# Kernel tuning notes

Measured on AMD Instinct MI355X. Metric: run time of the kernel, lower is better.

The kernel has to match this reference:

```python
import jax, jax.numpy as jnp
import numpy as np

NUM_HEADS = 8
HEAD_DIM = 64
AVG_K_LENGTH = 20
SCALE = 1.0 / (HEAD_DIM ** 0.5 * float(np.log(AVG_K_LENGTH)))  # 1/(sqrt(dim)*log(avg_k_length))


def setup_inputs() -> dict:
    key = jax.random.key(0)
    k1, k2, k3, k4 = jax.random.split(key, 4)
    B, HD, LQ, LK = 4, NUM_HEADS * HEAD_DIM, 2048, 2048
    q = jax.random.normal(k1, (B, HD, LQ), dtype=jnp.float32)
    k = jax.random.normal(k2, (B, HD, LK), dtype=jnp.float32)
    v = jax.random.normal(k3, (B, HD, LK), dtype=jnp.float32)
    k_length = jax.random.randint(k4, (B,), 512, LK + 1, dtype=jnp.int32)
    return {"q": q, "k": k, "v": v, "k_length": k_length}


def reference(q, k, v, k_length):
    b, hd, lq = q.shape
    lk = k.shape[-1]
    d = hd // NUM_HEADS
    # b (h d) l -> b h d l
    qh = q.reshape(b, NUM_HEADS, d, lq)
    kh = k.reshape(b, NUM_HEADS, d, lk)
    vh = v.reshape(b, NUM_HEADS, d, lk)
    # per-batch entropy-invariance scale: scale * log(k_length)
    s = SCALE * jnp.log(k_length.astype(jnp.float32))[:, None, None, None]  # (b,1,1,1)
    attn = jnp.einsum('bhdq,bhdk->bhqk', qh, kh)  # (b,h,lq,lk)
    attn = jax.nn.softmax(s * attn, axis=-1)
    out = jnp.einsum('bhqk,bhdk->bhdq', attn, vh)  # (b,h,d,lq)
    return out.reshape(b, hd, lq)
```

## Files before the change

### kernel.cpp

```cpp
#include <hip/hip_runtime.h>
#include <hip/hip_bf16.h>
#include <math.h>


typedef __attribute__((ext_vector_type(8))) short short8_t;
typedef __attribute__((ext_vector_type(4))) short short4_t;
typedef __attribute__((ext_vector_type(4))) float float4_t;

#define SEQ   2048
#define NBH   32
#define NKT   32

__device__ __forceinline__ unsigned f2bf2u(float a, float b) {
#if __has_builtin(__builtin_amdgcn_cvt_pk_bf16_f32)
  typedef __bf16 bf16x2_t __attribute__((ext_vector_type(2)));
  union { bf16x2_t v; unsigned u; } cv;
  cv.v = __builtin_amdgcn_cvt_pk_bf16_f32(a, b);
  return cv.u;
#else
  union { float f; unsigned u; } x, y;
  x.f = a; y.f = b;
  unsigned ra = x.u + 0x7fffu + ((x.u >> 16) & 1u);
  unsigned rb = y.u + 0x7fffu + ((y.u >> 16) & 1u);
  return (ra >> 16) | (rb & 0xffff0000u);
#endif
}

__device__ __forceinline__ short f2bf1(float a) {
  return (short)(f2bf2u(a, a) & 0xffffu);
}

__device__ __forceinline__ float fast_exp2(float x) {
#if __has_builtin(__builtin_amdgcn_exp2f)
  return __builtin_amdgcn_exp2f(x);
#else
  return exp2f(x);
#endif
}

__device__ __forceinline__ void gld16(const void* g, void* l) {
  __builtin_amdgcn_global_load_lds(
      (const __attribute__((address_space(1))) void*)g,
      (__attribute__((address_space(3))) void*)l, 16, 0, 0);
}

__device__ __forceinline__ float4_t mfma32(short8_t a, short8_t b, float4_t c) {
  return __builtin_amdgcn_mfma_f32_16x16x32_bf16(a, b, c, 0, 0, 0);
}

__device__ __forceinline__ float4_t mfma16(short4_t a, short4_t b, float4_t c) {
#if __has_builtin(__builtin_amdgcn_mfma_f32_16x16x16bf16_1k)
  return __builtin_amdgcn_mfma_f32_16x16x16bf16_1k(a, b, c, 0, 0, 0);
#else
  asm("v_mfma_f32_16x16x16_bf16 %0, %1, %2, %0" : "+v"(c) : "v"(a), "v"(b));
  return c;
#endif
}

#define PST 68
__global__ __launch_bounds__(256, 8)
void eia_prep_kernel(const float* __restrict__ kg, const float* __restrict__ vg,
                     unsigned short* __restrict__ Kt2, unsigned short* __restrict__ Vt2) {
  __shared__ __align__(16) short T[64 * PST];
  const int id  = blockIdx.x;
  const int isV = id >> 10;
  const int sub = id & 1023;
  const int bh  = sub >> 5;
  const int kt  = sub & 31;
  const int t   = threadIdx.x;

  if (!isV) {
    const size_t ib = ((size_t)bh * 64) * SEQ + (size_t)(kt * 64) + (t & 63);
    const int dg = t >> 6;
#pragma unroll
    for (int dd = 0; dd < 16; dd += 4) {
      const int d = dg * 16 + dd;
      const float f0 = kg[ib + (size_t)(d + 0) * SEQ];
      const float f1 = kg[ib + (size_t)(d + 1) * SEQ];
      const float f2 = kg[ib + (size_t)(d + 2) * SEQ];
      const float f3 = kg[ib + (size_t)(d + 3) * SEQ];
      union { short4_t s; unsigned u[2]; } p;
      p.u[0] = f2bf2u(f0, f1);
      p.u[1] = f2bf2u(f2, f3);
      *(short4_t*)&T[(t & 63) * PST + d] = p.s;
    }
    __syncthreads();
    unsigned short* outt = Kt2 + (size_t)(bh * 32 + kt) * 4096;
#pragma unroll
    for (int rep = 0; rep < 2; ++rep) {
      const int id2 = rep * 256 + t;
      const int lr = id2 & 63, ch = id2 >> 6;
      union { short8_t v; short4_t h[2]; } o;
      o.h[0] = *(const short4_t*)&T[lr * PST + ch * 8];
      o.h[1] = *(const short4_t*)&T[lr * PST + ch * 8 + 4];
      *(short8_t*)&outt[ch * 512 + lr * 8] = o.v;
    }
  } else {
#pragma unroll
    for (int rep = 0; rep < 4; ++rep) {
      const int id2 = rep * 256 + t;
      const int d = id2 >> 4, l4 = (id2 & 15) * 4;
      const float4_t f = *(const float4_t*)&vg[((size_t)bh * 64 + d) * SEQ + kt * 64 + l4];
      union { short4_t s; unsigned u[2]; } p;
      p.u[0] = f2bf2u(f[0], f[1]);
      p.u[1] = f2bf2u(f[2], f[3]);
      *(short4_t*)&T[d * PST + l4] = p.s;
    }
    __syncthreads();
    unsigned short* outt = Vt2 + (size_t)(bh * 32 + kt) * 4096;
#pragma unroll
    for (int rep = 0; rep < 2; ++rep) {
      const int c = rep * 256 + t;
      const int k4 = c >> 5, dp = c & 31;
      union { short8_t v; short4_t h[2]; } o;
      o.h[0] = *(const short4_t*)&T[(2 * dp) * PST + k4 * 4];
      o.h[1] = *(const short4_t*)&T[(2 * dp + 1) * PST + k4 * 4];
      *(short8_t*)&outt[k4 * 256 + dp * 8] = o.v;
    }
  }
}

__global__ __launch_bounds__(128, 2)
void eia_attn_kernel(const float* __restrict__ qg,
                     const unsigned short* __restrict__ Kt2,
                     const unsigned short* __restrict__ Vt2,
                     const int* __restrict__ klen,
                     float* __restrict__ outg) {
  __shared__ __align__(16) short SM[16384];

  const int tid  = threadIdx.x;
  const int bh   = blockIdx.x & 31;
  const int qt   = blockIdx.x >> 5;
  const int q0   = qt * 64;
  const int w    = tid >> 6;
  const int lane = tid & 63;
  const int quad = lane >> 4;
  const int l16  = lane & 15;

  const float c = (1.4426950408889634f / (8.0f * 2.9957322735539909f)) *
                  logf((float)klen[bh >> 3]);
  const size_t qb = (size_t)bh * 64 * SEQ;

#pragma unroll
  for (int rep = 0; rep < 8; ++rep) {
    const int id = rep * 128 + tid;
    const int d  = id >> 4;
    const int q4 = (id & 15) * 4;
    const float4_t f = *(const float4_t*)&qg[qb + (size_t)d * SEQ + (size_t)(q0 + q4)];
    SM[(q4 + 0) * 68 + d] = f2bf1(c * f[0]);
    SM[(q4 + 1) * 68 + d] = f2bf1(c * f[1]);
    SM[(q4 + 2) * 68 + d] = f2bf1(c * f[2]);
    SM[(q4 + 3) * 68 + d] = f2bf1(c * f[3]);
  }
  __syncthreads();

  short8_t qfrag[2][2];
#pragma unroll
  for (int g = 0; g < 2; ++g)
#pragma unroll
    for (int s = 0; s < 2; ++s) {
      const short* qp = &SM[(w * 32 + g * 16 + l16) * 68 + s * 32 + quad * 8];
      const short4_t lo = *(const short4_t*)qp;
      const short4_t hi = *(const short4_t*)(qp + 4);
      qfrag[g][s] = short8_t{lo[0], lo[1], lo[2], lo[3], hi[0], hi[1], hi[2], hi[3]};
    }
  __syncthreads();

  const char* ksrc = (const char*)Kt2 + (size_t)bh * NKT * 8192 + w * 4096 + lane * 16;
  const char* vsrc = (const char*)Vt2 + (size_t)bh * NKT * 8192 + w * 4096 + lane * 16;
  short* const kdst = &SM[w * 2048 + lane * 8];
  short* const vdst = &SM[8192 + w * 2048 + lane * 8];

  const short* const kfp = &SM[quad * 512 + l16 * 8];
  const short* const vfp = &SM[8192 + quad * 256 + l16 * 4];

  const float4_t z4 = {0.f, 0.f, 0.f, 0.f};
  float4_t oacc[2][4];
#pragma unroll
  for (int g = 0; g < 2; ++g)
#pragma unroll
    for (int tt = 0; tt < 4; ++tt) oacc[g][tt] = z4;
  float4_t lacc[2] = {z4, z4};
  const short one_bf = (short)0x3F80;
  const short4_t ones4 = (l16 == 0) ? short4_t{one_bf, one_bf, one_bf, one_bf}
                                    : short4_t{0, 0, 0, 0};

#pragma unroll
  for (int i = 0; i < 4; ++i) gld16(ksrc + i * 1024, kdst + i * 512);
#pragma unroll
  for (int i = 0; i < 4; ++i) gld16(vsrc + i * 1024, vdst + i * 512);
  size_t goff = 8192;

#pragma unroll 2
  for (int kt = 0; kt < NKT; ++kt) {
    __syncthreads();

    if (kt < NKT - 1) {
      const int pn = ((kt + 1) & 1) * 4096;
#pragma unroll
      for (int i = 0; i < 4; ++i) gld16(ksrc + goff + i * 1024, kdst + pn + i * 512);
#pragma unroll
      for (int i = 0; i < 4; ++i) gld16(vsrc + goff + i * 1024, vdst + pn + i * 512);
      goff += 8192;
    }
    const int par = (kt & 1) * 4096;

    float4_t sac[2][4];
#pragma unroll
    for (int t = 0; t < 4; ++t) {
      const short8_t kv = *(const short8_t*)(kfp + par + t * 128);
      sac[0][t] = mfma32(kv, qfrag[0][0], z4);
      sac[1][t] = mfma32(kv, qfrag[1][0], z4);
    }
#pragma unroll
    for (int t = 0; t < 4; ++t) {
      const short8_t kv = *(const short8_t*)(kfp + par + 2048 + t * 128);
      sac[0][t] = mfma32(kv, qfrag[0][1], sac[0][t]);
      sac[1][t] = mfma32(kv, qfrag[1][1], sac[1][t]);
    }

    short4_t pbf[2][4];
#pragma unroll
    for (int g = 0; g < 2; ++g)
#pragma unroll
      for (int t = 0; t < 4; ++t) {
        const float e0 = fast_exp2(sac[g][t][0]);
        const float e1 = fast_exp2(sac[g][t][1]);
        const float e2 = fast_exp2(sac[g][t][2]);
        const float e3 = fast_exp2(sac[g][t][3]);
        union { short4_t s; unsigned u[2]; } p;
        p.u[0] = f2bf2u(e0, e1);
        p.u[1] = f2bf2u(e2, e3);
        pbf[g][t] = p.s;
        lacc[g] = mfma16(ones4, pbf[g][t], lacc[g]);
      }

#pragma unroll
    for (int t = 0; t < 4; ++t) {
      const short* vfb = vfp + par + t * 1024;
#pragma unroll
      for (int tt = 0; tt < 4; ++tt) {
        const short4_t vv = *(const short4_t*)(vfb + tt * 64);
        oacc[0][tt] = mfma16(vv, pbf[0][t], oacc[0][tt]);
        oacc[1][tt] = mfma16(vv, pbf[1][t], oacc[1][tt]);
      }
    }
  }

#pragma unroll
  for (int g = 0; g < 2; ++g) {
    const float ls  = __shfl(lacc[g][0], l16, 64);
    const float inv = 1.0f / ls;
    const size_t ob = qb + (size_t)(q0 + w * 32 + g * 16 + l16);
#pragma unroll
    for (int tt = 0; tt < 4; ++tt)
#pragma unroll
      for (int r = 0; r < 4; ++r)
        outg[ob + (size_t)(tt * 16 + quad * 4 + r) * SEQ] = oacc[g][tt][r] * inv;
  }
}

#define DPAD  72
#define PPAD  68
__global__ __launch_bounds__(256, 5)
void eia_attn_fb(const float* __restrict__ qg, const float* __restrict__ kg,
                 const float* __restrict__ vg, const int* __restrict__ klen,
                 float* __restrict__ outg) {
  __shared__ __align__(16) short QPs[64 * DPAD];
  __shared__ __align__(16) short Ksf[64 * DPAD];
  __shared__ __align__(16) short Vsf[64 * DPAD];

  const int tid  = threadIdx.x;
  const int bh   = blockIdx.x & 31;
  const int qt   = blockIdx.x >> 5;
  const int q0   = qt * 64;
  const int w    = tid >> 6;
  const int lane = tid & 63;
  const int quad = lane >> 4;
  const int l16  = lane & 15;

  const size_t base = (size_t)bh * 64 * SEQ;
  const float c = (1.4426950408889634f / (8.0f * 2.9957322735539909f)) *
                  logf((float)klen[bh >> 3]);

#pragma unroll
  for (int it = 0; it < 2; ++it) {
    const int e = it * 4 + w;
    float f[8];
#pragma unroll
    for (int j = 0; j < 8; ++j)
      f[j] = c * qg[base + (size_t)(e * 8 + j) * SEQ + (size_t)(q0 + lane)];
    union { short8_t s8; unsigned u[4]; } t;
#pragma unroll
    for (int j = 0; j < 4; ++j) t.u[j] = f2bf2u(f[2 * j], f[2 * j + 1]);
    *(short8_t*)&QPs[lane * DPAD + e * 8] = t.s8;
  }
  __syncthreads();

  short8_t qfrag[2];
#pragma unroll
  for (int s = 0; s < 2; ++s)
    qfrag[s] = *(const short8_t*)&QPs[(w * 16 + l16) * DPAD + s * 32 + quad * 8];

  float4_t oacc[4];
#pragma unroll
  for (int t = 0; t < 4; ++t) { oacc[t][0] = 0.f; oacc[t][1] = 0.f; oacc[t][2] = 0.f; oacc[t][3] = 0.f; }
  float lsumv[4] = {0.f, 0.f, 0.f, 0.f};
  const int pbase = w * (16 * DPAD);

  for (int kt = 0; kt < NKT; ++kt) {
    const int k0 = kt * 64;
#pragma unroll
    for (int it = 0; it < 2; ++it) {
      float f[8];
#pragma unroll
      for (int j = 0; j < 8; ++j)
        f[j] = kg[base + (size_t)((it * 4 + w) * 8 + j) * SEQ + (size_t)(k0 + lane)];
      union { short8_t s8; unsigned u[4]; } t;
#pragma unroll
      for (int j = 0; j < 4; ++j) t.u[j] = f2bf2u(f[2 * j], f[2 * j + 1]);
      *(short8_t*)&Ksf[lane * DPAD + (it * 4 + w) * 8] = t.s8;
    }
#pragma unroll
    for (int it = 0; it < 4; ++it) {
      const int d = it * 16 + (w << 2) + (lane >> 4);
      const float4_t vv = *(const float4_t*)&vg[base + (size_t)d * SEQ + (size_t)(k0 + ((lane & 15) << 2))];
      union { short4_t s4; unsigned u[2]; } t;
      t.u[0] = f2bf2u(vv[0], vv[1]);
      t.u[1] = f2bf2u(vv[2], vv[3]);
      *(short4_t*)&Vsf[d * DPAD + ((lane & 15) << 2)] = t.s4;
    }
    __syncthreads();

    float4_t sacc[4];
#pragma unroll
    for (int t = 0; t < 4; ++t) { sacc[t][0] = 0.f; sacc[t][1] = 0.f; sacc[t][2] = 0.f; sacc[t][3] = 0.f; }
#pragma unroll
    for (int t = 0; t < 4; ++t)
#pragma unroll
      for (int s = 0; s < 2; ++s) {
        const short8_t bf = *(const short8_t*)&Ksf[(t * 16 + l16) * DPAD + s * 32 + quad * 8];
        sacc[t] = mfma32(qfrag[s], bf, sacc[t]);
      }

#pragma unroll
    for (int r = 0; r < 4; ++r) {
      const float p0 = fast_exp2(sacc[0][r]);
      const float p1 = fast_exp2(sacc[1][r]);
      const float p2 = fast_exp2(sacc[2][r]);
      const float p3 = fast_exp2(sacc[3][r]);
      lsumv[r] += (p0 + p1) + (p2 + p3);
      const int prow = pbase + (quad * 4 + r) * PPAD + l16;
      QPs[prow +  0] = f2bf1(p0);
      QPs[prow + 16] = f2bf1(p1);
      QPs[prow + 32] = f2bf1(p2);
      QPs[prow + 48] = f2bf1(p3);
    }

#pragma unroll
    for (int s = 0; s < 2; ++s) {
      const short* pr = &QPs[pbase + l16 * PPAD + s * 32 + quad * 8];
      const short4_t plo = *(const short4_t*)pr;
      const short4_t phi = *(const short4_t*)(pr + 4);
      const short8_t pf = {plo[0], plo[1], plo[2], plo[3], phi[0], phi[1], phi[2], phi[3]};
#pragma unroll
      for (int t = 0; t < 4; ++t) {
        const short8_t vf = *(const short8_t*)&Vsf[(t * 16 + l16) * DPAD + s * 32 + quad * 8];
        oacc[t] = mfma32(pf, vf, oacc[t]);
      }
    }
    __syncthreads();
  }

  float inv[4];
#pragma unroll
  for (int r = 0; r < 4; ++r) {
    float v = lsumv[r];
    v += __shfl_xor(v, 1);
    v += __shfl_xor(v, 2);
    v += __shfl_xor(v, 4);
    v += __shfl_xor(v, 8);
    inv[r] = 1.0f / v;
  }
#pragma unroll
  for (int t = 0; t < 4; ++t)
#pragma unroll
    for (int r = 0; r < 4; ++r)
      outg[base + (size_t)(t * 16 + l16) * SEQ +
           (size_t)(q0 + w * 16 + quad * 4 + r)] = oacc[t][r] * inv[r];
}

extern "C" void kernel_launch(void* const* d_in, const int* in_sizes, int n_in,
                              void* d_out, int out_size, void* d_ws, size_t ws_size,
                              hipStream_t stream) {
  const float* q  = (const float*)d_in[0];
  const float* k  = (const float*)d_in[1];
  const float* v  = (const float*)d_in[2];
  const int*   kl = (const int*)d_in[3];
  float* out = (float*)d_out;

  const size_t TEN  = (size_t)NBH * SEQ * 64;
  const size_t need = 2 * TEN * sizeof(unsigned short);

  if (ws_size >= need) {
    unsigned short* Kt2 = (unsigned short*)d_ws;
    unsigned short* Vt2 = Kt2 + TEN;
    eia_prep_kernel<<<2048, 256, 0, stream>>>(k, v, Kt2, Vt2);
    eia_attn_kernel<<<1024, 128, 0, stream>>>(q, Kt2, Vt2, kl, out);
  } else {
    eia_attn_fb<<<1024, 256, 0, stream>>>(q, k, v, kl, out);
  }
}
```

Measured before the change: 150.3 us.

## Double query tile per block and triple-buffer K/V with vmcnt-based waits

The attention kernel now runs four waves per block over 128 queries instead of two waves over 64. Each K/V tile staged in LDS is therefore reused by twice as many queries, halving block count and global/L2 K/V traffic. The LDS pipeline becomes a three-stage ring buffer with two tiles prefetched ahead. The full __syncthreads is replaced by explicit s_waitcnt vmcnt plus s_barrier, letting loads overlap more compute. LDS use grows to 48KB per block, which may limit occupancy, and the hand-written wait counts depend on the exact number of outstanding loads.

Result: faster. 139.8 us (-7.0%).

```diff
diff --git a/kernel.cpp b/kernel.cpp
--- a/kernel.cpp
+++ b/kernel.cpp
@@ -120,18 +120,18 @@
   }
 }
 
-__global__ __launch_bounds__(128, 2)
+__global__ __launch_bounds__(256, 2)
 void eia_attn_kernel(const float* __restrict__ qg,
                      const unsigned short* __restrict__ Kt2,
                      const unsigned short* __restrict__ Vt2,
                      const int* __restrict__ klen,
                      float* __restrict__ outg) {
-  __shared__ __align__(16) short SM[16384];
+  __shared__ __align__(16) short SM[24576];
 
   const int tid  = threadIdx.x;
   const int bh   = blockIdx.x & 31;
   const int qt   = blockIdx.x >> 5;
-  const int q0   = qt * 64;
+  const int q0   = qt * 128;
   const int w    = tid >> 6;
   const int lane = tid & 63;
   const int quad = lane >> 4;
@@ -143,9 +143,9 @@
 
 #pragma unroll
   for (int rep = 0; rep < 8; ++rep) {
-    const int id = rep * 128 + tid;
-    const int d  = id >> 4;
-    const int q4 = (id & 15) * 4;
+    const int id = rep * 256 + tid;
+    const int d  = id >> 5;
+    const int q4 = (id & 31) * 4;
     const float4_t f = *(const float4_t*)&qg[qb + (size_t)d * SEQ + (size_t)(q0 + q4)];
     SM[(q4 + 0) * 68 + d] = f2bf1(c * f[0]);
     SM[(q4 + 1) * 68 + d] = f2bf1(c * f[1]);
@@ -166,13 +166,13 @@
     }
   __syncthreads();
 
-  const char* ksrc = (const char*)Kt2 + (size_t)bh * NKT * 8192 + w * 4096 + lane * 16;
-  const char* vsrc = (const char*)Vt2 + (size_t)bh * NKT * 8192 + w * 4096 + lane * 16;
-  short* const kdst = &SM[w * 2048 + lane * 8];
-  short* const vdst = &SM[8192 + w * 2048 + lane * 8];
+  const char* ksrc = (const char*)Kt2 + (size_t)bh * NKT * 8192 + (2 * w) * 1024 + lane * 16;
+  const char* vsrc = (const char*)Vt2 + (size_t)bh * NKT * 8192 + (2 * w) * 1024 + lane * 16;
+  short* const kdst = &SM[(2 * w) * 512];
+  short* const vdst = &SM[12288 + (2 * w) * 512];
 
   const short* const kfp = &SM[quad * 512 + l16 * 8];
-  const short* const vfp = &SM[8192 + quad * 256 + l16 * 4];
+  const short* const vfp = &SM[12288 + quad * 256 + l16 * 4];
 
   const float4_t z4 = {0.f, 0.f, 0.f, 0.f};
   float4_t oacc[2][4];
@@ -185,36 +185,42 @@
   const short4_t ones4 = (l16 == 0) ? short4_t{one_bf, one_bf, one_bf, one_bf}
                                     : short4_t{0, 0, 0, 0};
 
-#pragma unroll
-  for (int i = 0; i < 4; ++i) gld16(ksrc + i * 1024, kdst + i * 512);
-#pragma unroll
-  for (int i = 0; i < 4; ++i) gld16(vsrc + i * 1024, vdst + i * 512);
-  size_t goff = 8192;
-
-#pragma unroll 2
+  gld16(ksrc, kdst);              gld16(ksrc + 1024, kdst + 512);
+  gld16(vsrc, vdst);              gld16(vsrc + 1024, vdst + 512);
+  gld16(ksrc + 8192, kdst + 4096); gld16(ksrc + 8192 + 1024, kdst + 4096 + 512);
+  gld16(vsrc + 8192, vdst + 4096); gld16(vsrc + 8192 + 1024, vdst + 4096 + 512);
+
+  int  sc = 0;
+  int  sn = 2;
+  size_t gsrc = 2 * 8192;
+
   for (int kt = 0; kt < NKT; ++kt) {
-    __syncthreads();
-
-    if (kt < NKT - 1) {
-      const int pn = ((kt + 1) & 1) * 4096;
-#pragma unroll
-      for (int i = 0; i < 4; ++i) gld16(ksrc + goff + i * 1024, kdst + pn + i * 512);
-#pragma unroll
-      for (int i = 0; i < 4; ++i) gld16(vsrc + goff + i * 1024, vdst + pn + i * 512);
-      goff += 8192;
-    }
-    const int par = (kt & 1) * 4096;
+    if (kt < NKT - 1) asm volatile("s_waitcnt vmcnt(4)" ::: "memory");
+    else              asm volatile("s_waitcnt vmcnt(0)" ::: "memory");
+    asm volatile("s_barrier" ::: "memory");
+
+    if (kt < NKT - 2) {
+      const int so = sn * 4096;
+      gld16(ksrc + gsrc, kdst + so); gld16(ksrc + gsrc + 1024, kdst + so + 512);
+      gld16(vsrc + gsrc, vdst + so); gld16(vsrc + gsrc + 1024, vdst + so + 512);
+      gsrc += 8192;
+      sn = (sn == 2) ? 0 : sn + 1;
+    }
+    const int koff = sc * 4096;
+    sc = (sc == 2) ? 0 : sc + 1;
+    const short* const kb = kfp + koff;
+    const short* const vb = vfp + koff;
 
     float4_t sac[2][4];
 #pragma unroll
     for (int t = 0; t < 4; ++t) {
-      const short8_t kv = *(const short8_t*)(kfp + par + t * 128);
+      const short8_t kv = *(const short8_t*)(kb + t * 128);
       sac[0][t] = mfma32(kv, qfrag[0][0], z4);
       sac[1][t] = mfma32(kv, qfrag[1][0], z4);
     }
 #pragma unroll
     for (int t = 0; t < 4; ++t) {
-      const short8_t kv = *(const short8_t*)(kfp + par + 2048 + t * 128);
+      const short8_t kv = *(const short8_t*)(kb + 2048 + t * 128);
       sac[0][t] = mfma32(kv, qfrag[0][1], sac[0][t]);
       sac[1][t] = mfma32(kv, qfrag[1][1], sac[1][t]);
     }
@@ -237,7 +243,7 @@
 
 #pragma unroll
     for (int t = 0; t < 4; ++t) {
-      const short* vfb = vfp + par + t * 1024;
+      const short* vfb = vb + t * 1024;
 #pragma unroll
       for (int tt = 0; tt < 4; ++tt) {
         const short4_t vv = *(const short4_t*)(vfb + tt * 64);
@@ -406,7 +412,7 @@
     unsigned short* Kt2 = (unsigned short*)d_ws;
     unsigned short* Vt2 = Kt2 + TEN;
     eia_prep_kernel<<<2048, 256, 0, stream>>>(k, v, Kt2, Vt2);
-    eia_attn_kernel<<<1024, 128, 0, stream>>>(q, Kt2, Vt2, kl, out);
+    eia_attn_kernel<<<512, 256, 0, stream>>>(q, Kt2, Vt2, kl, out);
   } else {
     eia_attn_fb<<<1024, 256, 0, stream>>>(q, k, v, kl, out);
   }
```

## Split key range across blocks with 128-query tiles and combine partial outputs

Applied to the files above, without the earlier changes.

Each block now holds 128 queries across 4 waves, with the K/V tile loads shared among the 4 waves so each global fetch serves twice as many queries. The key dimension is split in two halves handled by separate blocks, which write unnormalized partial outputs and row sums to workspace. A new combine kernel adds the halves and divides by the summed denominators. This keeps the grid at 1024 blocks while cutting K/V traffic per query, at the cost of an extra kernel launch and a full read/write pass over the output plus partials.

Result: faster. 146.7 us (-2.4%).

```diff
diff --git a/kernel.cpp b/kernel.cpp
--- a/kernel.cpp
+++ b/kernel.cpp
@@ -120,18 +120,23 @@
   }
 }
 
-__global__ __launch_bounds__(128, 2)
+template <int SPLIT>
+__global__ __launch_bounds__(256, SPLIT ? 4 : 2)
 void eia_attn_kernel(const float* __restrict__ qg,
                      const unsigned short* __restrict__ Kt2,
                      const unsigned short* __restrict__ Vt2,
                      const int* __restrict__ klen,
-                     float* __restrict__ outg) {
+                     float* __restrict__ outg,
+                     float* __restrict__ o1,
+                     float* __restrict__ lsink) {
   __shared__ __align__(16) short SM[16384];
 
   const int tid  = threadIdx.x;
   const int bh   = blockIdx.x & 31;
-  const int qt   = blockIdx.x >> 5;
-  const int q0   = qt * 64;
+  const int kh   = SPLIT ? ((blockIdx.x >> 5) & 1) : 0;
+  const int qt   = SPLIT ? (blockIdx.x >> 6) : (blockIdx.x >> 5);
+  const int NIT  = SPLIT ? 16 : 32;
+  const int q0   = qt * 128;
   const int w    = tid >> 6;
   const int lane = tid & 63;
   const int quad = lane >> 4;
@@ -143,9 +148,9 @@
 
 #pragma unroll
   for (int rep = 0; rep < 8; ++rep) {
-    const int id = rep * 128 + tid;
-    const int d  = id >> 4;
-    const int q4 = (id & 15) * 4;
+    const int id = rep * 256 + tid;
+    const int d  = id >> 5;
+    const int q4 = (id & 31) * 4;
     const float4_t f = *(const float4_t*)&qg[qb + (size_t)d * SEQ + (size_t)(q0 + q4)];
     SM[(q4 + 0) * 68 + d] = f2bf1(c * f[0]);
     SM[(q4 + 1) * 68 + d] = f2bf1(c * f[1]);
@@ -166,10 +171,11 @@
     }
   __syncthreads();
 
-  const char* ksrc = (const char*)Kt2 + (size_t)bh * NKT * 8192 + w * 4096 + lane * 16;
-  const char* vsrc = (const char*)Vt2 + (size_t)bh * NKT * 8192 + w * 4096 + lane * 16;
-  short* const kdst = &SM[w * 2048 + lane * 8];
-  short* const vdst = &SM[8192 + w * 2048 + lane * 8];
+  const size_t tbase = (size_t)bh * NKT * 8192 + (size_t)kh * (NKT / 2) * 8192 * SPLIT;
+  const char* ksrc = (const char*)Kt2 + tbase + (2 * w) * 1024 + lane * 16;
+  const char* vsrc = (const char*)Vt2 + tbase + (2 * w) * 1024 + lane * 16;
+  short* const kdst = &SM[(2 * w) * 512];
+  short* const vdst = &SM[8192 + (2 * w) * 512];
 
   const short* const kfp = &SM[quad * 512 + l16 * 8];
   const short* const vfp = &SM[8192 + quad * 256 + l16 * 4];
@@ -185,22 +191,18 @@
   const short4_t ones4 = (l16 == 0) ? short4_t{one_bf, one_bf, one_bf, one_bf}
                                     : short4_t{0, 0, 0, 0};
 
-#pragma unroll
-  for (int i = 0; i < 4; ++i) gld16(ksrc + i * 1024, kdst + i * 512);
-#pragma unroll
-  for (int i = 0; i < 4; ++i) gld16(vsrc + i * 1024, vdst + i * 512);
+  gld16(ksrc, kdst);  gld16(ksrc + 1024, kdst + 512);
+  gld16(vsrc, vdst);  gld16(vsrc + 1024, vdst + 512);
   size_t goff = 8192;
 
 #pragma unroll 2
-  for (int kt = 0; kt < NKT; ++kt) {
+  for (int kt = 0; kt < NIT; ++kt) {
     __syncthreads();
 
-    if (kt < NKT - 1) {
+    if (kt < NIT - 1) {
       const int pn = ((kt + 1) & 1) * 4096;
-#pragma unroll
-      for (int i = 0; i < 4; ++i) gld16(ksrc + goff + i * 1024, kdst + pn + i * 512);
-#pragma unroll
-      for (int i = 0; i < 4; ++i) gld16(vsrc + goff + i * 1024, vdst + pn + i * 512);
+      gld16(ksrc + goff, kdst + pn);       gld16(ksrc + goff + 1024, kdst + pn + 512);
+      gld16(vsrc + goff, vdst + pn);       gld16(vsrc + goff + 1024, vdst + pn + 512);
       goff += 8192;
     }
     const int par = (kt & 1) * 4096;
@@ -247,17 +249,51 @@
     }
   }
 
-#pragma unroll
-  for (int g = 0; g < 2; ++g) {
-    const float ls  = __shfl(lacc[g][0], l16, 64);
-    const float inv = 1.0f / ls;
-    const size_t ob = qb + (size_t)(q0 + w * 32 + g * 16 + l16);
-#pragma unroll
-    for (int tt = 0; tt < 4; ++tt)
-#pragma unroll
-      for (int r = 0; r < 4; ++r)
-        outg[ob + (size_t)(tt * 16 + quad * 4 + r) * SEQ] = oacc[g][tt][r] * inv;
-  }
+  if (SPLIT) {
+    float* const po = kh ? o1 : outg;
+    if (lane < 16) {
+      float* ls = lsink + (size_t)kh * (NBH * SEQ) + (size_t)bh * SEQ + q0 + w * 32 + lane;
+      ls[0]  = lacc[0][0];
+      ls[16] = lacc[1][0];
+    }
+#pragma unroll
+    for (int g = 0; g < 2; ++g) {
+      const size_t ob = qb + (size_t)(q0 + w * 32 + g * 16 + l16);
+#pragma unroll
+      for (int tt = 0; tt < 4; ++tt)
+#pragma unroll
+        for (int r = 0; r < 4; ++r)
+          po[ob + (size_t)(tt * 16 + quad * 4 + r) * SEQ] = oacc[g][tt][r];
+    }
+  } else {
+#pragma unroll
+    for (int g = 0; g < 2; ++g) {
+      const float ls  = __shfl(lacc[g][0], l16, 64);
+      const float inv = 1.0f / ls;
+      const size_t ob = qb + (size_t)(q0 + w * 32 + g * 16 + l16);
+#pragma unroll
+      for (int tt = 0; tt < 4; ++tt)
+#pragma unroll
+        for (int r = 0; r < 4; ++r)
+          outg[ob + (size_t)(tt * 16 + quad * 4 + r) * SEQ] = oacc[g][tt][r] * inv;
+    }
+  }
+}
+
+__global__ __launch_bounds__(256, 8)
+void eia_combine_kernel(float* __restrict__ outg, const float* __restrict__ o1,
+                        const float* __restrict__ lsink) {
+  const size_t j = ((size_t)blockIdx.x * 256 + threadIdx.x) * 4;
+  const int q  = (int)(j & (SEQ - 1));
+  const int bh = (int)(j >> 17);
+  const float4_t a  = *(const float4_t*)&outg[j];
+  const float4_t b  = *(const float4_t*)&o1[j];
+  const float4_t l0 = *(const float4_t*)&lsink[(size_t)bh * SEQ + q];
+  const float4_t l1 = *(const float4_t*)&lsink[(size_t)(NBH * SEQ) + (size_t)bh * SEQ + q];
+  float4_t r;
+#pragma unroll
+  for (int i = 0; i < 4; ++i) r[i] = (a[i] + b[i]) / (l0[i] + l1[i]);
+  *(float4_t*)&outg[j] = r;
 }
 
 #define DPAD  72
@@ -399,14 +435,25 @@
   const int*   kl = (const int*)d_in[3];
   float* out = (float*)d_out;
 
-  const size_t TEN  = (size_t)NBH * SEQ * 64;
-  const size_t need = 2 * TEN * sizeof(unsigned short);
-
-  if (ws_size >= need) {
+  const size_t TEN      = (size_t)NBH * SEQ * 64;
+  const size_t kv_bytes = 2 * TEN * sizeof(unsigned short);
+  const size_t o1_bytes = TEN * sizeof(float);
+  const size_t ls_bytes = 2 * (size_t)NBH * SEQ * sizeof(float);
+  const size_t need_split = kv_bytes + o1_bytes + ls_bytes;
+
+  if (ws_size >= need_split) {
+    unsigned short* Kt2 = (unsigned short*)d_ws;
+    unsigned short* Vt2 = Kt2 + TEN;
+    float* o1    = (float*)(Vt2 + TEN);
+    float* lsink = o1 + TEN;
+    eia_prep_kernel<<<2048, 256, 0, stream>>>(k, v, Kt2, Vt2);
+    eia_attn_kernel<1><<<1024, 256, 0, stream>>>(q, Kt2, Vt2, kl, out, o1, lsink);
+    eia_combine_kernel<<<(int)(TEN / 1024), 256, 0, stream>>>(out, o1, lsink);
+  } else if (ws_size >= kv_bytes) {
     unsigned short* Kt2 = (unsigned short*)d_ws;
     unsigned short* Vt2 = Kt2 + TEN;
     eia_prep_kernel<<<2048, 256, 0, stream>>>(k, v, Kt2, Vt2);
-    eia_attn_kernel<<<1024, 128, 0, stream>>>(q, Kt2, Vt2, kl, out);
+    eia_attn_kernel<0><<<512, 256, 0, stream>>>(q, Kt2, Vt2, kl, out, nullptr, nullptr);
   } else {
     eia_attn_fb<<<1024, 256, 0, stream>>>(q, k, v, kl, out);
   }
```
